# Kernel tuning notes

Measured on AMD Instinct MI355X. Metric: run time of the kernel, lower is better.

Reference implementation:

```python
import jax, jax.numpy as jnp
from jax import lax
import numpy as np

B, T, LAT, HID, OUT, NC = 1024, 128, 128, 256, 128, 2
HODE = 128          # ODEFunc hidden width (hard-coded 128 in source)
H = LAT // 2        # LSTM hidden = latent_dim / 2


def setup_inputs() -> dict:
    key = jax.random.key(0)
    ks = jax.random.split(key, 8)
    s = 0.05
    f32 = jnp.float32
    return {
        "initial_state": jax.random.normal(ks[0], (B, LAT), f32),
        "time_steps": jnp.linspace(0.0, 1.0, T, dtype=f32),
        "ode_w1": jax.random.normal(ks[1], (HODE, LAT), f32) * s,
        "ode_b1": jnp.zeros((HODE,), f32),
        "ode_w2": jax.random.normal(ks[2], (LAT, HODE), f32) * s,
        "ode_b2": jnp.zeros((LAT,), f32),
        "l2h_w": jax.random.normal(ks[3], (HID, LAT), f32) * s,
        "l2h_b": jnp.zeros((HID,), f32),
        "h2o_w": jax.random.normal(ks[4], (OUT, HID), f32) * s,
        "h2o_b": jnp.zeros((OUT,), f32),
        "lstm_wih": jax.random.normal(ks[5], (4 * H, LAT), f32) * s,
        "lstm_whh": jax.random.normal(ks[6], (4 * H, H), f32) * s,
        "lstm_bih": jnp.zeros((4 * H,), f32),
        "lstm_bhh": jnp.zeros((4 * H,), f32),
        "fc2_w": jax.random.normal(ks[7], (NC, H), f32) * s,
        "fc2_b": jnp.zeros((NC,), f32),
    }


def reference(initial_state, time_steps, ode_w1, ode_b1, ode_w2, ode_b2,
              l2h_w, l2h_b, h2o_w, h2o_b,
              lstm_wih, lstm_whh, lstm_bih, lstm_bhh, fc2_w, fc2_b):
    def ode_f(y):  # Linear-ELU-Linear, time-independent
        return jax.nn.elu(y @ ode_w1.T + ode_b1) @ ode_w2.T + ode_b2

    def rk4_step(y, dt):
        k1 = ode_f(y)
        k2 = ode_f(y + 0.5 * dt * k1)
        k3 = ode_f(y + 0.5 * dt * k2)
        k4 = ode_f(y + dt * k3)
        y_new = y + (dt / 6.0) * (k1 + 2.0 * k2 + 2.0 * k3 + k4)
        return y_new, y_new

    dts = time_steps[1:] - time_steps[:-1]
    _, ys = lax.scan(rk4_step, initial_state, dts)
    zs = jnp.concatenate([initial_state[None], ys], axis=0)  # [T, B, LAT] = odeint output

    # torch: cat((initial_state.unsqueeze(0), zs)).permute(1,0,2) -> [B, T+1, LAT]
    input_lstm = jnp.concatenate([initial_state[None], zs], axis=0).transpose(1, 0, 2)

    # nn.LSTM is seq-first, so it scans dim0 (=B) with dim1 (=T+1) as its batch.
    h0 = jnp.zeros((input_lstm.shape[1], H), input_lstm.dtype)
    c0 = jnp.zeros_like(h0)

    def cell(carry, x):
        h, c = carry
        gates = x @ lstm_wih.T + lstm_bih + h @ lstm_whh.T + lstm_bhh
        i, f, g, o = jnp.split(gates, 4, axis=-1)  # torch gate order i,f,g,o
        c = jax.nn.sigmoid(f) * c + jax.nn.sigmoid(i) * jnp.tanh(g)
        h = jax.nn.sigmoid(o) * jnp.tanh(c)
        return (h, c), h

    _, lstm_hs = lax.scan(cell, (h0, c0), input_lstm)  # [B, T+1, H]
    lstm_out = lstm_hs[:, -1, :] @ fc2_w.T + fc2_b      # [B, NC]

    hs = zs @ l2h_w.T + l2h_b   # [T, B, HID]
    xs = hs @ h2o_w.T + h2o_b   # [T, B, OUT]
    return xs, lstm_out
```

## Files before the change

### kernel.cpp

```cpp
#include <hip/hip_runtime.h>


typedef short s16x8 __attribute__((ext_vector_type(8)));
typedef float f32x4 __attribute__((ext_vector_type(4)));
typedef _Float16 f16x2 __attribute__((ext_vector_type(2)));
typedef _Float16 f16x8 __attribute__((ext_vector_type(8)));

#define MFMA16(a, b, c) __builtin_amdgcn_mfma_f32_16x16x32_bf16((a), (b), (c), 0, 0, 0)

__device__ __forceinline__ void lds_barrier() {
  asm volatile("s_waitcnt lgkmcnt(0)\n\ts_barrier" ::: "memory");
}

__device__ __forceinline__ unsigned short f2bf(float x) {
  union { float f; unsigned u; } v; v.f = x;
  return (unsigned short)((v.u + 0x7FFFu + ((v.u >> 16) & 1u)) >> 16);
}

__device__ __forceinline__ unsigned cvtpk(float lo, float hi) {
  unsigned r;
  asm("v_cvt_pk_bf16_f32 %0, %1, %2" : "=v"(r) : "v"(lo), "v"(hi));
  return r;
}

__device__ __forceinline__ int swz(int row, int col2) {
  return row * 256 + (col2 ^ ((row & 7) << 4));
}

__device__ __forceinline__ f16x8 cvt8(const float* p) {
  float4 a = *(const float4*)p, b = *(const float4*)(p + 4);
  return (f16x8){(_Float16)a.x, (_Float16)a.y, (_Float16)a.z, (_Float16)a.w,
                 (_Float16)b.x, (_Float16)b.y, (_Float16)b.z, (_Float16)b.w};
}

__global__ __launch_bounds__(128) void wf_kernel(
    const float* __restrict__ h2o, const float* __restrict__ l2h,
    const float* __restrict__ l2hb, const float* __restrict__ h2ob,
    unsigned short* __restrict__ wfo, float* __restrict__ bfo)
{
  const int o = (int)blockIdx.x, k = (int)threadIdx.x;
  float acc = 0.f;
  for (int h = 0; h < 256; ++h) acc = fmaf(h2o[o * 256 + h], l2h[h * 128 + k], acc);
  wfo[o * 128 + k] = f2bf(acc);
  __shared__ float red[128];
  red[k] = h2o[o * 256 + k] * l2hb[k] + h2o[o * 256 + 128 + k] * l2hb[128 + k];
  __syncthreads();
  for (int s = 64; s > 0; s >>= 1) {
    if (k < s) red[k] += red[k + s];
    __syncthreads();
  }
  if (k == 0) bfo[o] = red[0] + h2ob[o];
}

__global__ __launch_bounds__(256, 1) void ode_kernel(
    const float* __restrict__ init, const float* __restrict__ ts,
    const float* __restrict__ w1, const float* __restrict__ b1,
    const float* __restrict__ w2, const float* __restrict__ b2,
    const unsigned short* __restrict__ wf, const float* __restrict__ bfv_,
    const float* __restrict__ wih, const float* __restrict__ bih,
    const float* __restrict__ bhh,
    float* __restrict__ xs, float* __restrict__ XW4)
{
  __shared__ __align__(16) unsigned char sY[4096];
  __shared__ __align__(16) unsigned char sH[4096];
  __shared__ __align__(16) float sYf[2048];
  const int tid = (int)threadIdx.x;
  const int w = tid >> 6, lane = tid & 63;
  const int l15 = lane & 15, l4 = lane >> 4;
  const int rowbase = (int)blockIdx.x * 16;
  const int colbase = w * 32;

  s16x8 w1f[2][4], w2f[2][4], wff[2][4];
#pragma unroll
  for (int tc = 0; tc < 2; ++tc) {
    const int rj = colbase + 16 * tc + l15;
#pragma unroll
    for (int ks = 0; ks < 4; ++ks) {
      const int kb = ks * 32 + l4 * 8;
      s16x8 va, vb;
#pragma unroll
      for (int t = 0; t < 8; ++t) {
        va[t] = (short)f2bf(w1[rj * 128 + kb + t]);
        vb[t] = (short)f2bf(w2[rj * 128 + kb + t]);
      }
      w1f[tc][ks] = va; w2f[tc][ks] = vb;
      wff[tc][ks] = *(const s16x8*)(wf + rj * 128 + kb);
    }
  }
  float b1v[2], b2v[2], bv[2];
#pragma unroll
  for (int tc = 0; tc < 2; ++tc) {
    const int cc = colbase + 16 * tc + l15;
    b1v[tc] = b1[cc]; b2v[tc] = b2[cc]; bv[tc] = bfv_[cc];
  }

  int aOff[4];
#pragma unroll
  for (int ks = 0; ks < 4; ++ks) aOff[ks] = swz(l15, (ks * 32 + l4 * 8) * 2);
  int cOff[2][4];
#pragma unroll
  for (int tc = 0; tc < 2; ++tc)
#pragma unroll
    for (int r = 0; r < 4; ++r)
      cOff[tc][r] = swz(l4 * 4 + r, (colbase + 16 * tc + l15) * 2);

  float y0[2][4], yac[2][4];
#pragma unroll
  for (int tc = 0; tc < 2; ++tc)
#pragma unroll
    for (int r = 0; r < 4; ++r)
      y0[tc][r] = init[(rowbase + l4 * 4 + r) * 128 + colbase + 16 * tc + l15];

  {
    const int i = tid * 8;
    const int row = i >> 7, col = i & 127;
    union { unsigned short u[8]; s16x8 v; } p;
#pragma unroll
    for (int t = 0; t < 8; ++t) p.u[t] = f2bf(init[(rowbase + row) * 128 + col + t]);
    *(s16x8*)(sY + swz(row, col * 2)) = p.v;
  }
  __syncthreads();

  float* xsp = xs + (long)(rowbase + l4 * 4) * 128 + colbase + l15;
  const f32x4 fz = {0.f, 0.f, 0.f, 0.f};

  for (int s = 0; s < 127; ++s) {
    const float dt = ts[s + 1] - ts[s];
    const float c16 = dt * (1.f / 6.f), c13 = dt * (1.f / 3.f), ch = dt * 0.5f;
#pragma unroll
    for (int st = 0; st < 4; ++st) {
      f32x4 acc[2];
      acc[0] = fz; acc[1] = fz;
      if (st == 0) {
        s16x8 a[4];
#pragma unroll
        for (int ks = 0; ks < 4; ++ks) a[ks] = *(const s16x8*)(sY + aOff[ks]);
        f32x4 pa[2];
        pa[0] = fz; pa[1] = fz;
#pragma unroll
        for (int ks = 0; ks < 4; ++ks) {
          acc[0] = MFMA16(a[ks], w1f[0][ks], acc[0]);
          acc[1] = MFMA16(a[ks], w1f[1][ks], acc[1]);
          pa[0] = MFMA16(a[ks], wff[0][ks], pa[0]);
          pa[1] = MFMA16(a[ks], wff[1][ks], pa[1]);
        }
#pragma unroll
        for (int tc = 0; tc < 2; ++tc)
#pragma unroll
          for (int r = 0; r < 4; ++r)
            xsp[r * 128 + tc * 16] = pa[tc][r] + bv[tc];
        xsp += 131072;
      } else {
#pragma unroll
        for (int ks = 0; ks < 4; ++ks) {
          s16x8 a = *(const s16x8*)(sY + aOff[ks]);
          acc[0] = MFMA16(a, w1f[0][ks], acc[0]);
          acc[1] = MFMA16(a, w1f[1][ks], acc[1]);
        }
      }
#pragma unroll
      for (int r = 0; r < 4; ++r) {
        float v0 = acc[0][r] + b1v[0];
        float v1 = acc[1][r] + b1v[1];
        v0 = v0 > 0.f ? v0 : (__expf(v0) - 1.f);
        v1 = v1 > 0.f ? v1 : (__expf(v1) - 1.f);
        const unsigned p = cvtpk(v0, v1);
        *(unsigned short*)(sH + cOff[0][r]) = (unsigned short)p;
        *(unsigned short*)(sH + cOff[1][r]) = (unsigned short)(p >> 16);
      }
      lds_barrier();
      f32x4 kc[2];
      kc[0] = fz; kc[1] = fz;
#pragma unroll
      for (int ks = 0; ks < 4; ++ks) {
        s16x8 a = *(const s16x8*)(sH + aOff[ks]);
        kc[0] = MFMA16(a, w2f[0][ks], kc[0]);
        kc[1] = MFMA16(a, w2f[1][ks], kc[1]);
      }
#pragma unroll
      for (int r = 0; r < 4; ++r) {
        float yn2[2];
#pragma unroll
        for (int tc = 0; tc < 2; ++tc) {
          const float kv = kc[tc][r] + b2v[tc];
          float yn;
          if (st == 0)      { yac[tc][r] = fmaf(c16, kv, y0[tc][r]);  yn = fmaf(ch, kv, y0[tc][r]); }
          else if (st == 1) { yac[tc][r] = fmaf(c13, kv, yac[tc][r]); yn = fmaf(ch, kv, y0[tc][r]); }
          else if (st == 2) { yac[tc][r] = fmaf(c13, kv, yac[tc][r]); yn = fmaf(dt, kv, y0[tc][r]); }
          else              { y0[tc][r]  = fmaf(c16, kv, yac[tc][r]); yn = y0[tc][r]; }
          yn2[tc] = yn;
        }
        const unsigned p = cvtpk(yn2[0], yn2[1]);
        *(unsigned short*)(sY + cOff[0][r]) = (unsigned short)p;
        *(unsigned short*)(sY + cOff[1][r]) = (unsigned short)(p >> 16);
      }
      lds_barrier();
    }
  }
  {
    f32x4 pa[2];
    pa[0] = fz; pa[1] = fz;
#pragma unroll
    for (int ks = 0; ks < 4; ++ks) {
      s16x8 a = *(const s16x8*)(sY + aOff[ks]);
      pa[0] = MFMA16(a, wff[0][ks], pa[0]);
      pa[1] = MFMA16(a, wff[1][ks], pa[1]);
    }
#pragma unroll
    for (int tc = 0; tc < 2; ++tc)
#pragma unroll
      for (int r = 0; r < 4; ++r)
        xsp[r * 128 + tc * 16] = pa[tc][r] + bv[tc];
  }
#pragma unroll
  for (int tc = 0; tc < 2; ++tc)
#pragma unroll
    for (int r = 0; r < 4; ++r)
      sYf[(l4 * 4 + r) * 128 + colbase + 16 * tc + l15] = y0[tc][r];
  lds_barrier();
  {
    const int g = tid;
    const int q = g >> 6, j = g & 63;
#pragma unroll 4
    for (int tl = 0; tl < 16; ++tl) {
      float a0 = 0.f, a1 = 0.f, a2 = 0.f, a3 = 0.f;
#pragma unroll 8
      for (int k = 0; k < 32; ++k) {
        float4 wv = *(const float4*)(wih + g * 128 + 4 * k);
        float4 yv = *(const float4*)(sYf + tl * 128 + 4 * k);
        a0 = fmaf(wv.x, yv.x, a0); a1 = fmaf(wv.y, yv.y, a1);
        a2 = fmaf(wv.z, yv.z, a2); a3 = fmaf(wv.w, yv.w, a3);
      }
      XW4[(rowbase + tl) * 256 + j * 4 + q] = bih[g] + bhh[g] + ((a0 + a1) + (a2 + a3));
    }
  }
}

__global__ __launch_bounds__(256, 1) void lstm_kernel(
    const float* __restrict__ XW4,
    const float* __restrict__ whh,
    float* __restrict__ hsT)
{
  const int tid = (int)threadIdx.x;
  const int L = tid & 63;
  const int q = L & 3;
  const int j = (tid >> 6) * 16 + (L >> 2);
  const int row = q * 64 + j;

  __shared__ __align__(16) _Float16 hbuf[2][64];

  f16x8 wq[8];
#pragma unroll
  for (int k = 0; k < 8; ++k) wq[k] = cvt8(whh + row * 64 + 8 * k);

  const float Aa = (q == 2) ? 2.f : 1.f;
  const float Sa = (q == 2) ? -2.f : -1.f;
  const float Ba = (q == 2) ? -1.f : 0.f;

  if (tid < 64) hbuf[0][tid] = (_Float16)0.f;
  float c = 0.f;

  const int xwi = j * 4 + q;
  float xq[4];
#pragma unroll
  for (int i = 0; i < 4; ++i) xq[i] = XW4[i * 256 + xwi];
  lds_barrier();

  for (int tb = 0; tb < 256; ++tb) {
#pragma unroll
    for (int i = 0; i < 4; ++i) {
      const int t = tb * 4 + i;
      const int cur = i & 1;
      const float xw = xq[i];
      xq[i] = XW4[((t + 4) & 1023) * 256 + xwi];

      const f16x8* hb8 = (const f16x8*)hbuf[cur];
      float4 ac = {0.f, 0.f, 0.f, 0.f};
#pragma unroll
      for (int r = 0; r < 8; ++r) {
        const f16x8 v = hb8[r];
        ac.x = __builtin_amdgcn_fdot2(__builtin_shufflevector(wq[r], wq[r], 0, 1),
                                      __builtin_shufflevector(v, v, 0, 1), ac.x, false);
        ac.y = __builtin_amdgcn_fdot2(__builtin_shufflevector(wq[r], wq[r], 2, 3),
                                      __builtin_shufflevector(v, v, 2, 3), ac.y, false);
        ac.z = __builtin_amdgcn_fdot2(__builtin_shufflevector(wq[r], wq[r], 4, 5),
                                      __builtin_shufflevector(v, v, 4, 5), ac.z, false);
        ac.w = __builtin_amdgcn_fdot2(__builtin_shufflevector(wq[r], wq[r], 6, 7),
                                      __builtin_shufflevector(v, v, 6, 7), ac.w, false);
      }
      const float pre = xw + ((ac.x + ac.y) + (ac.z + ac.w));
      const float act = fmaf(Aa, __builtin_amdgcn_rcpf(1.f + __expf(Sa * pre)), Ba);

      const int ai = __float_as_int(act);
      const float x1 = __int_as_float(__builtin_amdgcn_mov_dpp(ai, 0xB1, 0xF, 0xF, true));
      const float x2 = __int_as_float(__builtin_amdgcn_mov_dpp(ai, 0x4E, 0xF, 0xF, true));
      const float x3 = __int_as_float(__builtin_amdgcn_mov_dpp(ai, 0x1B, 0xF, 0xF, true));
      const float gi = (q == 0) ? act : (q == 1) ? x1 : (q == 2) ? x2 : x3;
      const float gf = (q == 0) ? x1 : (q == 1) ? act : (q == 2) ? x3 : x2;
      const float gg = (q == 0) ? x2 : (q == 1) ? x3 : (q == 2) ? act : x1;
      const float go = (q == 0) ? x3 : (q == 1) ? x2 : (q == 2) ? x1 : act;

      c = fmaf(gf, c, gi * gg);
      const float th = fmaf(2.f, __builtin_amdgcn_rcpf(1.f + __expf(-2.f * c)), -1.f);
      const float h = go * th;

      if (q == 0) {
        hbuf[cur ^ 1][j] = (_Float16)h;
        hsT[j * 1024 + t] = h;
      }
      lds_barrier();
    }
  }
}

__global__ __launch_bounds__(256) void fc2_kernel(
    const float* __restrict__ hsT, const float* __restrict__ fw,
    const float* __restrict__ fb, float* __restrict__ lout)
{
  const int idx = (int)blockIdx.x * 256 + (int)threadIdx.x;
  const int n = idx >> 10, t = idx & 1023;
  float acc = fb[n];
#pragma unroll 8
  for (int j = 0; j < 64; ++j) acc = fmaf(fw[n * 64 + j], hsT[j * 1024 + t], acc);
  lout[t * 2 + n] = acc;
}

extern "C" void kernel_launch(void* const* d_in, const int* in_sizes, int n_in,
                              void* d_out, int out_size, void* d_ws, size_t ws_size,
                              hipStream_t stream) {
  const float* init  = (const float*)d_in[0];
  const float* ts    = (const float*)d_in[1];
  const float* ode_w1 = (const float*)d_in[2];
  const float* ode_b1 = (const float*)d_in[3];
  const float* ode_w2 = (const float*)d_in[4];
  const float* ode_b2 = (const float*)d_in[5];
  const float* l2h_w = (const float*)d_in[6];
  const float* l2h_b = (const float*)d_in[7];
  const float* h2o_w = (const float*)d_in[8];
  const float* h2o_b = (const float*)d_in[9];
  const float* wih   = (const float*)d_in[10];
  const float* whh   = (const float*)d_in[11];
  const float* bih   = (const float*)d_in[12];
  const float* bhh   = (const float*)d_in[13];
  const float* fc2w  = (const float*)d_in[14];
  const float* fc2b  = (const float*)d_in[15];

  char* ws = (char*)d_ws;
  float* XW4            = (float*)(ws);
  float* hsT            = (float*)(ws + 1048576);
  unsigned short* wfbuf = (unsigned short*)(ws + 1310720);
  float* bfused         = (float*)(ws + 1343488);

  float* xs   = (float*)d_out;
  float* lout = xs + 16777216;

  wf_kernel<<<128, 128, 0, stream>>>(h2o_w, l2h_w, l2h_b, h2o_b, wfbuf, bfused);
  ode_kernel<<<64, 256, 0, stream>>>(init, ts, ode_w1, ode_b1, ode_w2, ode_b2,
                                     wfbuf, bfused, wih, bih, bhh, xs, XW4);
  lstm_kernel<<<1, 256, 0, stream>>>(XW4, whh, hsT);
  fc2_kernel<<<8, 256, 0, stream>>>(hsT, fc2w, fc2b, lout);
}
```

Measured before the change: 701.3 us.

## Move output projection out of ODE loop into kernel overlapped with LSTM

The ODE kernel stops computing the fused h2o·l2h projection inside its RK4 loop. It now writes each bf16 state to a workspace buffer. A new combined kernel runs the single-block LSTM recurrence in block 0, while 2048 other blocks compute the projection from that buffer, so the projection overlaps the serial LSTM. This shortens the serial critical path of the ODE loop but adds 32 MB of global writes and reads. It also widens the LDS swizzle to 16 rows and splits the LSTM dot-product accumulators to shorten dependency chains.

```diff
diff --git a/kernel.cpp b/kernel.cpp
--- a/kernel.cpp
+++ b/kernel.cpp
@@ -24,7 +24,7 @@
 }
 
 __device__ __forceinline__ int swz(int row, int col2) {
-  return row * 256 + (col2 ^ ((row & 7) << 4));
+  return row * 256 + (col2 ^ ((row & 15) << 4));
 }
 
 __device__ __forceinline__ f16x8 cvt8(const float* p) {
@@ -33,33 +33,13 @@
                  (_Float16)b.x, (_Float16)b.y, (_Float16)b.z, (_Float16)b.w};
 }
 
-__global__ __launch_bounds__(128) void wf_kernel(
-    const float* __restrict__ h2o, const float* __restrict__ l2h,
-    const float* __restrict__ l2hb, const float* __restrict__ h2ob,
-    unsigned short* __restrict__ wfo, float* __restrict__ bfo)
-{
-  const int o = (int)blockIdx.x, k = (int)threadIdx.x;
-  float acc = 0.f;
-  for (int h = 0; h < 256; ++h) acc = fmaf(h2o[o * 256 + h], l2h[h * 128 + k], acc);
-  wfo[o * 128 + k] = f2bf(acc);
-  __shared__ float red[128];
-  red[k] = h2o[o * 256 + k] * l2hb[k] + h2o[o * 256 + 128 + k] * l2hb[128 + k];
-  __syncthreads();
-  for (int s = 64; s > 0; s >>= 1) {
-    if (k < s) red[k] += red[k + s];
-    __syncthreads();
-  }
-  if (k == 0) bfo[o] = red[0] + h2ob[o];
-}
-
 __global__ __launch_bounds__(256, 1) void ode_kernel(
     const float* __restrict__ init, const float* __restrict__ ts,
     const float* __restrict__ w1, const float* __restrict__ b1,
     const float* __restrict__ w2, const float* __restrict__ b2,
-    const unsigned short* __restrict__ wf, const float* __restrict__ bfv_,
     const float* __restrict__ wih, const float* __restrict__ bih,
     const float* __restrict__ bhh,
-    float* __restrict__ xs, float* __restrict__ XW4)
+    unsigned short* __restrict__ zbuf, float* __restrict__ XW4)
 {
   __shared__ __align__(16) unsigned char sY[4096];
   __shared__ __align__(16) unsigned char sH[4096];
@@ -70,7 +50,7 @@
   const int rowbase = (int)blockIdx.x * 16;
   const int colbase = w * 32;
 
-  s16x8 w1f[2][4], w2f[2][4], wff[2][4];
+  s16x8 w1f[2][4], w2f[2][4];
 #pragma unroll
   for (int tc = 0; tc < 2; ++tc) {
     const int rj = colbase + 16 * tc + l15;
@@ -84,14 +64,13 @@
         vb[t] = (short)f2bf(w2[rj * 128 + kb + t]);
       }
       w1f[tc][ks] = va; w2f[tc][ks] = vb;
-      wff[tc][ks] = *(const s16x8*)(wf + rj * 128 + kb);
-    }
-  }
-  float b1v[2], b2v[2], bv[2];
+    }
+  }
+  float b1v[2], b2v[2];
 #pragma unroll
   for (int tc = 0; tc < 2; ++tc) {
     const int cc = colbase + 16 * tc + l15;
-    b1v[tc] = b1[cc]; b2v[tc] = b2[cc]; bv[tc] = bfv_[cc];
+    b1v[tc] = b1[cc]; b2v[tc] = b2[cc];
   }
 
   int aOff[4];
@@ -118,10 +97,10 @@
 #pragma unroll
     for (int t = 0; t < 8; ++t) p.u[t] = f2bf(init[(rowbase + row) * 128 + col + t]);
     *(s16x8*)(sY + swz(row, col * 2)) = p.v;
+    *(s16x8*)(zbuf + rowbase * 128 + i) = p.v;
   }
   __syncthreads();
 
-  float* xsp = xs + (long)(rowbase + l4 * 4) * 128 + colbase + l15;
   const f32x4 fz = {0.f, 0.f, 0.f, 0.f};
 
   for (int s = 0; s < 127; ++s) {
@@ -131,32 +110,11 @@
     for (int st = 0; st < 4; ++st) {
       f32x4 acc[2];
       acc[0] = fz; acc[1] = fz;
-      if (st == 0) {
-        s16x8 a[4];
-#pragma unroll
-        for (int ks = 0; ks < 4; ++ks) a[ks] = *(const s16x8*)(sY + aOff[ks]);
-        f32x4 pa[2];
-        pa[0] = fz; pa[1] = fz;
-#pragma unroll
-        for (int ks = 0; ks < 4; ++ks) {
-          acc[0] = MFMA16(a[ks], w1f[0][ks], acc[0]);
-          acc[1] = MFMA16(a[ks], w1f[1][ks], acc[1]);
-          pa[0] = MFMA16(a[ks], wff[0][ks], pa[0]);
-          pa[1] = MFMA16(a[ks], wff[1][ks], pa[1]);
-        }
-#pragma unroll
-        for (int tc = 0; tc < 2; ++tc)
-#pragma unroll
-          for (int r = 0; r < 4; ++r)
-            xsp[r * 128 + tc * 16] = pa[tc][r] + bv[tc];
-        xsp += 131072;
-      } else {
-#pragma unroll
-        for (int ks = 0; ks < 4; ++ks) {
-          s16x8 a = *(const s16x8*)(sY + aOff[ks]);
-          acc[0] = MFMA16(a, w1f[0][ks], acc[0]);
-          acc[1] = MFMA16(a, w1f[1][ks], acc[1]);
-        }
+#pragma unroll
+      for (int ks = 0; ks < 4; ++ks) {
+        s16x8 a = *(const s16x8*)(sY + aOff[ks]);
+        acc[0] = MFMA16(a, w1f[0][ks], acc[0]);
+        acc[1] = MFMA16(a, w1f[1][ks], acc[1]);
       }
 #pragma unroll
       for (int r = 0; r < 4; ++r) {
@@ -196,21 +154,12 @@
       }
       lds_barrier();
     }
-  }
-  {
-    f32x4 pa[2];
-    pa[0] = fz; pa[1] = fz;
-#pragma unroll
-    for (int ks = 0; ks < 4; ++ks) {
-      s16x8 a = *(const s16x8*)(sY + aOff[ks]);
-      pa[0] = MFMA16(a, wff[0][ks], pa[0]);
-      pa[1] = MFMA16(a, wff[1][ks], pa[1]);
-    }
-#pragma unroll
-    for (int tc = 0; tc < 2; ++tc)
-#pragma unroll
-      for (int r = 0; r < 4; ++r)
-        xsp[r * 128 + tc * 16] = pa[tc][r] + bv[tc];
+    {
+      const int i = tid * 8;
+      const int row = i >> 7;
+      const s16x8 v = *(const s16x8*)(sY + swz(row, (i & 127) * 2));
+      *(s16x8*)(zbuf + (long)(s + 1) * 131072 + rowbase * 128 + i) = v;
+    }
   }
 #pragma unroll
   for (int tc = 0; tc < 2; ++tc)
@@ -236,7 +185,71 @@
   }
 }
 
-__global__ __launch_bounds__(256, 1) void lstm_kernel(
+__global__ __launch_bounds__(128) void wf_kernel(
+    const float* __restrict__ h2o, const float* __restrict__ l2h,
+    const float* __restrict__ l2hb, const float* __restrict__ h2ob,
+    unsigned short* __restrict__ wfo, float* __restrict__ bfo)
+{
+  const int o = (int)blockIdx.x, k = (int)threadIdx.x;
+  float acc = 0.f;
+  for (int h = 0; h < 256; ++h) acc = fmaf(h2o[o * 256 + h], l2h[h * 128 + k], acc);
+  wfo[o * 128 + k] = f2bf(acc);
+  __shared__ float red[128];
+  red[k] = h2o[o * 256 + k] * l2hb[k] + h2o[o * 256 + 128 + k] * l2hb[128 + k];
+  __syncthreads();
+  for (int s = 64; s > 0; s >>= 1) {
+    if (k < s) red[k] += red[k + s];
+    __syncthreads();
+  }
+  if (k == 0) bfo[o] = red[0] + h2ob[o];
+}
+
+__device__ __forceinline__ void proj_body(
+    const unsigned short* __restrict__ zbuf, const unsigned short* __restrict__ wf,
+    const float* __restrict__ bfv_, float* __restrict__ xs)
+{
+  const int tid = (int)threadIdx.x;
+  const int w = tid >> 6, lane = tid & 63;
+  const int l15 = lane & 15, l4 = lane >> 4;
+  const int colbase = w * 32;
+  const long rowbase = (long)(blockIdx.x - 1) * 64;
+
+  s16x8 wff[2][4];
+#pragma unroll
+  for (int tc = 0; tc < 2; ++tc) {
+    const int rj = colbase + 16 * tc + l15;
+#pragma unroll
+    for (int ks = 0; ks < 4; ++ks)
+      wff[tc][ks] = *(const s16x8*)(wf + rj * 128 + ks * 32 + l4 * 8);
+  }
+  const float bv0 = bfv_[colbase + l15], bv1 = bfv_[colbase + 16 + l15];
+
+  const f32x4 fz = {0.f, 0.f, 0.f, 0.f};
+  f32x4 acc[4][2];
+#pragma unroll
+  for (int rt = 0; rt < 4; ++rt) { acc[rt][0] = fz; acc[rt][1] = fz; }
+
+#pragma unroll
+  for (int rt = 0; rt < 4; ++rt) {
+    const long rb = rowbase + rt * 16 + l15;
+#pragma unroll
+    for (int ks = 0; ks < 4; ++ks) {
+      const s16x8 a = *(const s16x8*)(zbuf + rb * 128 + ks * 32 + l4 * 8);
+      acc[rt][0] = MFMA16(a, wff[0][ks], acc[rt][0]);
+      acc[rt][1] = MFMA16(a, wff[1][ks], acc[rt][1]);
+    }
+  }
+#pragma unroll
+  for (int rt = 0; rt < 4; ++rt)
+#pragma unroll
+    for (int r = 0; r < 4; ++r) {
+      const long row = rowbase + rt * 16 + l4 * 4 + r;
+      xs[row * 128 + colbase + l15]      = acc[rt][0][r] + bv0;
+      xs[row * 128 + colbase + 16 + l15] = acc[rt][1][r] + bv1;
+    }
+}
+
+__device__ __forceinline__ void lstm_body(
     const float* __restrict__ XW4,
     const float* __restrict__ whh,
     float* __restrict__ hsT)
@@ -275,10 +288,11 @@
       xq[i] = XW4[((t + 4) & 1023) * 256 + xwi];
 
       const f16x8* hb8 = (const f16x8*)hbuf[cur];
-      float4 ac = {0.f, 0.f, 0.f, 0.f};
+      float4 ac0 = {0.f, 0.f, 0.f, 0.f}, ac1 = {0.f, 0.f, 0.f, 0.f};
 #pragma unroll
       for (int r = 0; r < 8; ++r) {
         const f16x8 v = hb8[r];
+        float4& ac = (r & 1) ? ac1 : ac0;
         ac.x = __builtin_amdgcn_fdot2(__builtin_shufflevector(wq[r], wq[r], 0, 1),
                                       __builtin_shufflevector(v, v, 0, 1), ac.x, false);
         ac.y = __builtin_amdgcn_fdot2(__builtin_shufflevector(wq[r], wq[r], 2, 3),
@@ -288,7 +302,8 @@
         ac.w = __builtin_amdgcn_fdot2(__builtin_shufflevector(wq[r], wq[r], 6, 7),
                                       __builtin_shufflevector(v, v, 6, 7), ac.w, false);
       }
-      const float pre = xw + ((ac.x + ac.y) + (ac.z + ac.w));
+      const float pre = xw + (((ac0.x + ac0.y) + (ac0.z + ac0.w)) +
+                              ((ac1.x + ac1.y) + (ac1.z + ac1.w)));
       const float act = fmaf(Aa, __builtin_amdgcn_rcpf(1.f + __expf(Sa * pre)), Ba);
 
       const int ai = __float_as_int(act);
@@ -311,6 +326,16 @@
       lds_barrier();
     }
   }
+}
+
+__global__ __launch_bounds__(256, 1) void proj_lstm_kernel(
+    const unsigned short* __restrict__ zbuf, const unsigned short* __restrict__ wf,
+    const float* __restrict__ bfv_, float* __restrict__ xs,
+    const float* __restrict__ XW4, const float* __restrict__ whh,
+    float* __restrict__ hsT)
+{
+  if (blockIdx.x == 0) lstm_body(XW4, whh, hsT);
+  else                 proj_body(zbuf, wf, bfv_, xs);
 }
 
 __global__ __launch_bounds__(256) void fc2_kernel(
@@ -346,17 +371,18 @@
   const float* fc2b  = (const float*)d_in[15];
 
   char* ws = (char*)d_ws;
-  float* XW4            = (float*)(ws);
-  float* hsT            = (float*)(ws + 1048576);
-  unsigned short* wfbuf = (unsigned short*)(ws + 1310720);
-  float* bfused         = (float*)(ws + 1343488);
+  unsigned short* zbuf  = (unsigned short*)(ws);
+  float* XW4            = (float*)(ws + 33554432);
+  float* hsT            = (float*)(ws + 34603008);
+  unsigned short* wfbuf = (unsigned short*)(ws + 34865152);
+  float* bfused         = (float*)(ws + 34897920);
 
   float* xs   = (float*)d_out;
   float* lout = xs + 16777216;
 
+  ode_kernel<<<64, 256, 0, stream>>>(init, ts, ode_w1, ode_b1, ode_w2, ode_b2,
+                                     wih, bih, bhh, zbuf, XW4);
   wf_kernel<<<128, 128, 0, stream>>>(h2o_w, l2h_w, l2h_b, h2o_b, wfbuf, bfused);
-  ode_kernel<<<64, 256, 0, stream>>>(init, ts, ode_w1, ode_b1, ode_w2, ode_b2,
-                                     wfbuf, bfused, wih, bih, bhh, xs, XW4);
-  lstm_kernel<<<1, 256, 0, stream>>>(XW4, whh, hsT);
+  proj_lstm_kernel<<<2049, 256, 0, stream>>>(zbuf, wfbuf, bfused, xs, XW4, whh, hsT);
   fc2_kernel<<<8, 256, 0, stream>>>(hsT, fc2w, fc2b, lout);
 }
```

After: 706.2 us (median of 2 runs). Within noise of the previous version (+0.7%).
